# Kernel optimization log

Hardware: AMD Instinct MI355X
Metric: run time of the kernel (lower is better)

## Reference

```python
import jax, jax.numpy as jnp
import numpy as np
import math

B, S, HID = 2, 2048, 4096
NH, NKV = 32, 8
HD = HID // NH  # 128
ROPE_BASE = 10000.0


def _rope_tables(seq_len, dim, base=ROPE_BASE):
    # ntk_alpha = 1 and mscale = 1 for seq_len <= training_seqlen
    inv_freq = 1.0 / (base ** (jnp.arange(0, dim, 2, dtype=jnp.float32) / dim))
    t = jnp.arange(seq_len, dtype=jnp.float32)
    freqs = jnp.einsum('i,j->ij', t, inv_freq)          # [S, dim/2]
    emb = jnp.concatenate([freqs, freqs], axis=-1)       # [S, dim]
    return jnp.cos(emb), jnp.sin(emb)


def setup_inputs() -> dict:
    key = jax.random.key(0)
    ks = jax.random.split(key, 5)
    hidden_states = jax.random.normal(ks[0], (B, S, HID), dtype=jnp.float32)
    # additive causal mask [B, 1, S, S]
    causal = jnp.where(jnp.tril(jnp.ones((S, S), dtype=bool)), 0.0, -1e9)
    attention_mask = jnp.broadcast_to(causal[None, None], (B, 1, S, S)).astype(jnp.float32)
    cos, sin = _rope_tables(S, HD)
    sc = 0.02
    Wq = jax.random.normal(ks[1], (HID, HID), dtype=jnp.float32) * sc
    Wkv = jax.random.normal(ks[2], (2 * NKV * HD, HID), dtype=jnp.float32) * sc
    Wd = jax.random.normal(ks[3], (HID, HID), dtype=jnp.float32) * sc
    bd = jnp.zeros((HID,), dtype=jnp.float32)
    return {"hidden_states": hidden_states, "attention_mask": attention_mask,
            "cos": cos, "sin": sin, "Wq": Wq, "Wkv": Wkv, "Wd": Wd, "bd": bd}


def _rotate_half(x):
    x1, x2 = jnp.split(x, 2, axis=-1)
    return jnp.concatenate([-x2, x1], axis=-1)


def reference(hidden_states, attention_mask, cos, sin, Wq, Wkv, Wd, bd):
    bsz, seq_len, _ = hidden_states.shape
    # Q projection: [B,S,HID] -> [B,NH,S,HD]
    q = (hidden_states @ Wq.T).reshape(bsz, seq_len, NH, HD).transpose(0, 2, 1, 3)
    # fused KV projection: [B,S,NKV,2*HD] -> split -> [B,NKV,S,HD] each
    kv = (hidden_states @ Wkv.T).reshape(bsz, seq_len, NKV, 2 * HD)
    k, v = jnp.split(kv, 2, axis=-1)
    k = k.transpose(0, 2, 1, 3)
    v = v.transpose(0, 2, 1, 3)
    # RoPE (broadcast cos/sin [S,HD] over batch and heads)
    c = cos[None, None, :, :]
    s = sin[None, None, :, :]
    q = q * c + _rotate_half(q) * s
    k = k * c + _rotate_half(k) * s
    # repeat_kv: expand KV heads to NH heads (group size NH//NKV)
    n_rep = NH // NKV
    k = jnp.repeat(k, n_rep, axis=1)  # [B,NH,S,HD]
    v = jnp.repeat(v, n_rep, axis=1)
    # attention
    scores = jnp.einsum('bhqd,bhkd->bhqk', q, k) / math.sqrt(HD)
    scores = scores + attention_mask[:, :, :, :seq_len]
    probs = jax.nn.softmax(scores.astype(jnp.float32), axis=-1).astype(q.dtype)
    attn = jnp.einsum('bhqk,bhkd->bhqd', probs, v)
    attn = attn.transpose(0, 2, 1, 3).reshape(bsz, seq_len, HID)
    return attn @ Wd.T + bd
```

## Files before the change

kernel.cpp:

```cpp
#include <hip/hip_runtime.h>

typedef __bf16 bf16;
typedef __bf16 bf16x4 __attribute__((ext_vector_type(4)));
typedef __bf16 bf16x8 __attribute__((ext_vector_type(8)));
typedef float floatx4 __attribute__((ext_vector_type(4)));

static constexpr int B_ = 2, S_ = 2048, HID_ = 4096, NH_ = 32, NKV_ = 8, HD_ = 128;

__device__ __forceinline__ void gll16(const void* g, void* l) {
    __builtin_amdgcn_global_load_lds(
        (const __attribute__((address_space(1))) void*)g,
        (__attribute__((address_space(3))) void*)l, 16, 0, 0);
}

__device__ __forceinline__ bf16x8 cvt8(const float* p) {
    float4 f0 = *(const float4*)p;
    float4 f1 = *(const float4*)(p + 4);
    bf16x8 v;
    v[0] = (bf16)f0.x; v[1] = (bf16)f0.y; v[2] = (bf16)f0.z; v[3] = (bf16)f0.w;
    v[4] = (bf16)f1.x; v[5] = (bf16)f1.y; v[6] = (bf16)f1.z; v[7] = (bf16)f1.w;
    return v;
}

__global__ __launch_bounds__(256) void cvt_kernel(const float* __restrict__ in,
                                                  bf16* __restrict__ out, int n8)
{
    int i = blockIdx.x * 256 + threadIdx.x;
    if (i >= n8) return;
    ((bf16x8*)out)[i] = cvt8(in + (size_t)i * 8);
}

template<bool ABF, bool WBF, int EPI>
__global__ __launch_bounds__(256) void gemm_kernel(
    const void* __restrict__ Ap, const void* __restrict__ Wp,
    const float* __restrict__ bias, void* __restrict__ Cp,
    bf16* __restrict__ Kw, bf16* __restrict__ Vtw,
    int M, int N, int K)
{
    constexpr bool FAST = ABF && WBF;
    constexpr int STR = FAST ? 32 : 40;
    __shared__ __attribute__((aligned(16))) bf16 smem[2 * 128 * 40];
    bf16* Als = smem;
    bf16* Bls = smem + 128 * STR;

    const int tid = threadIdx.x;
    const int lane = tid & 63, wave = tid >> 6;
    const int lm = lane & 15, lq = lane >> 4;
    const int wr = (wave >> 1) * 64, wc = (wave & 1) * 64;
    const int m0 = blockIdx.y * 128, n0 = blockIdx.x * 128;

    floatx4 acc[4][4];
    #pragma unroll
    for (int i = 0; i < 4; i++)
        #pragma unroll
        for (int j = 0; j < 4; j++) acc[i][j] = (floatx4){0.f, 0.f, 0.f, 0.f};

    const int sr = tid >> 1;
    const int sc = (tid & 1) * 16;

    for (int k0 = 0; k0 < K; k0 += 32) {
        __syncthreads();
        if (FAST) {
            #pragma unroll
            for (int t = 0; t < 2; t++) {
                const int o = wave * 2048 + t * 1024 + lane * 16;
                const int row = o >> 6, ch = (o >> 4) & 3;
                const int ub = wave * 1024 + t * 512;
                gll16((const bf16*)Ap + (size_t)(m0 + row) * K + k0 + ch * 8, &Als[ub]);
                gll16((const bf16*)Wp + (size_t)(n0 + row) * K + k0 + ch * 8, &Bls[ub]);
            }
        } else {
            if (ABF) {
                const bf16* aptr = (const bf16*)Ap + (size_t)(m0 + sr) * K + sc + k0;
                *(bf16x8*)&Als[sr * STR + sc]     = *(const bf16x8*)(aptr);
                *(bf16x8*)&Als[sr * STR + sc + 8] = *(const bf16x8*)(aptr + 8);
            } else {
                const float* aptr = (const float*)Ap + (size_t)(m0 + sr) * K + sc + k0;
                *(bf16x8*)&Als[sr * STR + sc]     = cvt8(aptr);
                *(bf16x8*)&Als[sr * STR + sc + 8] = cvt8(aptr + 8);
            }
            const float* wptr = (const float*)Wp + (size_t)(n0 + sr) * K + sc + k0;
            *(bf16x8*)&Bls[sr * STR + sc]     = cvt8(wptr);
            *(bf16x8*)&Bls[sr * STR + sc + 8] = cvt8(wptr + 8);
        }
        __syncthreads();
        bf16x8 af[4], bfr[4];
        const int ko = lq * 8;
        #pragma unroll
        for (int i = 0; i < 4; i++) af[i]  = *(const bf16x8*)&Als[(wr + i * 16 + lm) * STR + ko];
        #pragma unroll
        for (int j = 0; j < 4; j++) bfr[j] = *(const bf16x8*)&Bls[(wc + j * 16 + lm) * STR + ko];
        #pragma unroll
        for (int i = 0; i < 4; i++)
            #pragma unroll
            for (int j = 0; j < 4; j++)
                acc[i][j] = __builtin_amdgcn_mfma_f32_16x16x32_bf16(af[i], bfr[j], acc[i][j], 0, 0, 0);
    }

    #pragma unroll
    for (int i = 0; i < 4; i++)
        #pragma unroll
        for (int j = 0; j < 4; j++) {
            const int col = n0 + wc + j * 16 + lm;
            const int row0 = m0 + wr + i * 16 + lq * 4;
            if (EPI == 0) {
                #pragma unroll
                for (int r = 0; r < 4; r++)
                    ((bf16*)Cp)[(size_t)(row0 + r) * N + col] = (bf16)acc[i][j][r];
            } else if (EPI == 1) {
                const float bv = bias ? bias[col] : 0.f;
                #pragma unroll
                for (int r = 0; r < 4; r++)
                    ((float*)Cp)[(size_t)(row0 + r) * N + col] = acc[i][j][r] + bv;
            } else {
                const int head = col >> 8, off = col & 255;
                const int b = row0 >> 11, s0 = row0 & (S_ - 1);
                if (off < HD_) {
                    bf16* kp = Kw + ((size_t)(b * NKV_ + head) * S_ + s0) * HD_ + off;
                    #pragma unroll
                    for (int r = 0; r < 4; r++) kp[(size_t)r * HD_] = (bf16)acc[i][j][r];
                } else {
                    bf16x4 pv;
                    #pragma unroll
                    for (int r = 0; r < 4; r++) pv[r] = (bf16)acc[i][j][r];
                    *(bf16x4*)&Vtw[((size_t)(b * NKV_ + head) * HD_ + (off - HD_)) * S_ + s0] = pv;
                }
            }
        }
}

__global__ __launch_bounds__(256) void rope_kernel(
    bf16* __restrict__ Qd, bf16* __restrict__ Kd,
    const float* __restrict__ cosd, const float* __restrict__ sind)
{
    const int idx = blockIdx.x * 256 + threadIdx.x;
    const int QROWS = B_ * S_ * NH_;
    const int d = idx & 63;
    const int row = idx >> 6;
    bf16* base; int s;
    if (row < QROWS) { base = Qd + (size_t)row * HD_; s = (row / NH_) & (S_ - 1); }
    else            { int rk = row - QROWS; base = Kd + (size_t)rk * HD_; s = rk & (S_ - 1); }
    const float c  = cosd[s * HD_ + d];
    const float sn = sind[s * HD_ + d];
    const float x1 = (float)base[d];
    const float x2 = (float)base[d + 64];
    base[d]      = (bf16)(x1 * c - x2 * sn);
    base[d + 64] = (bf16)(x2 * c + x1 * sn);
}

__global__ __launch_bounds__(256) void attn_kernel(
    const bf16* __restrict__ Q, const bf16* __restrict__ Kw,
    const bf16* __restrict__ Vtw, bf16* __restrict__ O)
{
    const int bq = (int)gridDim.x - 1 - (int)blockIdx.x;
    const int h = blockIdx.y, b = blockIdx.z;
    const int kh = h >> 2;
    const int tid = threadIdx.x, wave = tid >> 6, lane = tid & 63;
    const int lm = lane & 15, lq = lane >> 4;

    __shared__ __attribute__((aligned(16))) bf16 Kls[64 * 128];
    __shared__ __attribute__((aligned(16))) bf16 Vls[128 * 64];
    __shared__ __attribute__((aligned(16))) bf16 Pls[4][16 * 72];

    const int q0 = bq * 64 + wave * 16;
    bf16x8 qa[4];
    {
        const bf16* qb = Q + ((size_t)(b * S_ + q0 + lm) * NH_ + h) * HD_;
        #pragma unroll
        for (int ks = 0; ks < 4; ks++) qa[ks] = *(const bf16x8*)(qb + ks * 32 + lq * 8);
    }

    float l_i[4];
    floatx4 oacc[8];
    #pragma unroll
    for (int r = 0; r < 4; r++) l_i[r] = 0.f;
    #pragma unroll
    for (int ct = 0; ct < 8; ct++) oacc[ct] = (floatx4){0.f, 0.f, 0.f, 0.f};

    const float scale = 0.08838834764831845f;
    const bf16* Kbase = Kw  + (size_t)(b * NKV_ + kh) * S_ * HD_;
    const bf16* Vbase = Vtw + (size_t)(b * NKV_ + kh) * HD_ * S_;
    const int nkt = bq + 1;

    for (int it = 0; it < nkt; ++it) {
        const int kt = it * 64;
        __syncthreads();
        #pragma unroll
        for (int t = 0; t < 4; t++) {
            const int o = wave * 4096 + t * 1024 + lane * 16;
            const int ub = (wave * 4096 + t * 1024) / 2;
            { const int row = o >> 8, pos = (o >> 4) & 15, c = (pos - row) & 15;
              gll16(Kbase + (size_t)(kt + row) * HD_ + c * 8, &Kls[ub]); }
            { const int row = o >> 7, pos = (o >> 4) & 7, c = (pos - row) & 7;
              gll16(Vbase + (size_t)row * S_ + kt + c * 8, &Vls[ub]); }
        }
        __syncthreads();

        floatx4 sacc[4];
        #pragma unroll
        for (int nt = 0; nt < 4; nt++) sacc[nt] = (floatx4){0.f, 0.f, 0.f, 0.f};
        #pragma unroll
        for (int nt = 0; nt < 4; nt++) {
            const int key = nt * 16 + lm;
            #pragma unroll
            for (int ks = 0; ks < 4; ks++) {
                bf16x8 kf = *(const bf16x8*)&Kls[key * 128 + ((ks * 4 + lq + key) & 15) * 8];
                sacc[nt] = __builtin_amdgcn_mfma_f32_16x16x32_bf16(qa[ks], kf, sacc[nt], 0, 0, 0);
            }
        }

        #pragma unroll
        for (int r = 0; r < 4; r++) {
            const int qrow = q0 + lq * 4 + r;
            float lacc = 0.f;
            #pragma unroll
            for (int nt = 0; nt < 4; nt++) {
                const int kcol = kt + nt * 16 + lm;
                const float sv = sacc[nt][r] * scale + (kcol > qrow ? -1e9f : 0.f);
                const float p = __expf(sv - 20.0f);
                lacc += p;
                Pls[wave][(lq * 4 + r) * 72 + nt * 16 + lm] = (bf16)p;
            }
            l_i[r] += lacc;
        }

        #pragma unroll
        for (int ks2 = 0; ks2 < 2; ks2++) {
            bf16x8 pa = *(const bf16x8*)&Pls[wave][lm * 72 + ks2 * 32 + lq * 8];
            #pragma unroll
            for (int ct = 0; ct < 8; ct++) {
                const int dr = ct * 16 + lm;
                bf16x8 vb = *(const bf16x8*)&Vls[dr * 64 + ((ks2 * 4 + lq + dr) & 7) * 8];
                oacc[ct] = __builtin_amdgcn_mfma_f32_16x16x32_bf16(pa, vb, oacc[ct], 0, 0, 0);
            }
        }
    }

    #pragma unroll
    for (int r = 0; r < 4; r++) {
        float l = l_i[r];
        #pragma unroll
        for (int off = 1; off < 16; off <<= 1)
            l += __shfl_xor(l, off, 64);
        l_i[r] = l;
    }

    #pragma unroll
    for (int ct = 0; ct < 8; ct++)
        #pragma unroll
        for (int r = 0; r < 4; r++) {
            const int qrow = q0 + lq * 4 + r;
            O[(size_t)(b * S_ + qrow) * HID_ + h * HD_ + ct * 16 + lm]
                = (bf16)(oacc[ct][r] / l_i[r]);
        }
}

extern "C" void kernel_launch(void* const* d_in, const int* in_sizes, int n_in,
                              void* d_out, int out_size, void* d_ws, size_t ws_size,
                              hipStream_t stream)
{
    const float* hidden = (const float*)d_in[0];
    const float* cosd = (const float*)d_in[2];
    const float* sind = (const float*)d_in[3];
    const float* Wq   = (const float*)d_in[4];
    const float* Wkv  = (const float*)d_in[5];
    const float* Wd   = (const float*)d_in[6];
    const float* bd   = (const float*)d_in[7];
    float* out = (float*)d_out;

    const int M = B_ * S_;
    const int NKVC = 2 * NKV_ * HD_;
    bf16* Qw = (bf16*)d_out;
    bf16* wsb = (bf16*)d_ws;
    dim3 blk(256);

    const size_t E_HID  = (size_t)M * HID_;
    const size_t E_WKV  = (size_t)NKVC * HID_;
    const size_t E_K    = (size_t)B_ * NKV_ * S_ * HD_;
    const bool full = ws_size >= 2 * (3 * E_HID + E_WKV + 2 * E_K);

    const int rope_blocks = (B_ * S_ * NH_ + B_ * NKV_ * S_) * 64 / 256;

    if (full) {
        bf16* hb   = wsb;
        bf16* wqb  = hb   + E_HID;
        bf16* wkvb = wqb  + E_HID;
        bf16* wdb  = wkvb + E_WKV;
        bf16* Kw   = wdb  + E_HID;
        bf16* Vtw  = Kw   + E_K;
        bf16* Aw   = hb;

        cvt_kernel<<<dim3(E_HID / 8 / 256), blk, 0, stream>>>(hidden, hb,  (int)(E_HID / 8));
        cvt_kernel<<<dim3(E_HID / 8 / 256), blk, 0, stream>>>(Wq,     wqb, (int)(E_HID / 8));
        cvt_kernel<<<dim3(E_WKV / 8 / 256), blk, 0, stream>>>(Wkv,    wkvb,(int)(E_WKV / 8));
        cvt_kernel<<<dim3(E_HID / 8 / 256), blk, 0, stream>>>(Wd,     wdb, (int)(E_HID / 8));

        gemm_kernel<true, true, 0><<<dim3(HID_ / 128, M / 128), blk, 0, stream>>>(
            hb, wqb, nullptr, Qw, nullptr, nullptr, M, HID_, HID_);
        gemm_kernel<true, true, 2><<<dim3(NKVC / 128, M / 128), blk, 0, stream>>>(
            hb, wkvb, nullptr, nullptr, Kw, Vtw, M, NKVC, HID_);
        rope_kernel<<<dim3(rope_blocks), blk, 0, stream>>>(Qw, Kw, cosd, sind);
        attn_kernel<<<dim3(S_ / 64, NH_, B_), blk, 0, stream>>>(Qw, Kw, Vtw, Aw);
        gemm_kernel<true, true, 1><<<dim3(HID_ / 128, M / 128), blk, 0, stream>>>(
            Aw, wdb, bd, out, nullptr, nullptr, M, HID_, HID_);
    } else {
        bf16* Kw  = wsb;
        bf16* Vtw = Kw  + E_K;
        bf16* Aw  = Vtw + E_K;

        gemm_kernel<false, false, 0><<<dim3(HID_ / 128, M / 128), blk, 0, stream>>>(
            hidden, Wq, nullptr, Qw, nullptr, nullptr, M, HID_, HID_);
        gemm_kernel<false, false, 2><<<dim3(NKVC / 128, M / 128), blk, 0, stream>>>(
            hidden, Wkv, nullptr, nullptr, Kw, Vtw, M, NKVC, HID_);
        rope_kernel<<<dim3(rope_blocks), blk, 0, stream>>>(Qw, Kw, cosd, sind);
        attn_kernel<<<dim3(S_ / 64, NH_, B_), blk, 0, stream>>>(Qw, Kw, Vtw, Aw);
        gemm_kernel<true, false, 1><<<dim3(HID_ / 128, M / 128), blk, 0, stream>>>(
            Aw, Wd, bd, out, nullptr, nullptr, M, HID_, HID_);
    }
}
```

Baseline: 1.009 ms.

## Replace bf16 GEMMs with 256x256-tile, 4-stage pipelined 512-thread kernel

Adds a new GEMM kernel with 256x256 output tiles, 8 waves per block, and a 4-slot LDS ring buffer. Tiles are prefetched three K-steps ahead with direct global-to-LDS loads under explicit vmcnt waits, and MFMA phases are interleaved with loads under raised priority. The three projection GEMMs in the full-workspace path now use it, aiming to hide memory latency and increase per-block data reuse. In exchange it uses much more LDS and registers, and with fewer, larger blocks (for example 256 for the Q and output GEMMs) occupancy and tail balance may suffer.

```diff
diff --git a/kernel.cpp b/kernel.cpp
--- a/kernel.cpp
+++ b/kernel.cpp
@@ -30,75 +30,108 @@
     ((bf16x8*)out)[i] = cvt8(in + (size_t)i * 8);
 }
 
-template<bool ABF, bool WBF, int EPI>
-__global__ __launch_bounds__(256) void gemm_kernel(
-    const void* __restrict__ Ap, const void* __restrict__ Wp,
+template<int EPI>
+__global__ __launch_bounds__(512, 2) void gemm256_kernel(
+    const bf16* __restrict__ Ap, const bf16* __restrict__ Wp,
     const float* __restrict__ bias, void* __restrict__ Cp,
     bf16* __restrict__ Kw, bf16* __restrict__ Vtw,
     int M, int N, int K)
 {
-    constexpr bool FAST = ABF && WBF;
-    constexpr int STR = FAST ? 32 : 40;
-    __shared__ __attribute__((aligned(16))) bf16 smem[2 * 128 * 40];
-    bf16* Als = smem;
-    bf16* Bls = smem + 128 * STR;
+    __shared__ __attribute__((aligned(16))) bf16 As[4 * 8192];
+    __shared__ __attribute__((aligned(16))) bf16 Bs[4 * 8192];
 
     const int tid = threadIdx.x;
-    const int lane = tid & 63, wave = tid >> 6;
+    const int lane = tid & 63, wv = tid >> 6;
     const int lm = lane & 15, lq = lane >> 4;
-    const int wr = (wave >> 1) * 64, wc = (wave & 1) * 64;
-    const int m0 = blockIdx.y * 128, n0 = blockIdx.x * 128;
-
-    floatx4 acc[4][4];
-    #pragma unroll
-    for (int i = 0; i < 4; i++)
+    const int wr = (wv >> 2) * 128, wc = (wv & 3) * 64;
+    const int m0 = blockIdx.y * 256, n0 = blockIdx.x * 256;
+
+    const int NT = K >> 5;
+
+    const int sr = lane >> 2, sch = lane & 3;
+    const bf16* aA0 = Ap + (size_t)(m0 + wv * 32 +      sr) * K + sch * 8;
+    const bf16* aA1 = Ap + (size_t)(m0 + wv * 32 + 16 + sr) * K + sch * 8;
+    const bf16* aB0 = Wp + (size_t)(n0 + wv * 32 +      sr) * K + sch * 8;
+    const bf16* aB1 = Wp + (size_t)(n0 + wv * 32 + 16 + sr) * K + sch * 8;
+    const int ub0 = wv * 1024;
+    const int ub1 = wv * 1024 + 512;
+
+    floatx4 acc[8][4];
+    #pragma unroll
+    for (int i = 0; i < 8; i++)
         #pragma unroll
         for (int j = 0; j < 4; j++) acc[i][j] = (floatx4){0.f, 0.f, 0.f, 0.f};
 
-    const int sr = tid >> 1;
-    const int sc = (tid & 1) * 16;
-
-    for (int k0 = 0; k0 < K; k0 += 32) {
-        __syncthreads();
-        if (FAST) {
-            #pragma unroll
-            for (int t = 0; t < 2; t++) {
-                const int o = wave * 2048 + t * 1024 + lane * 16;
-                const int row = o >> 6, ch = (o >> 4) & 3;
-                const int ub = wave * 1024 + t * 512;
-                gll16((const bf16*)Ap + (size_t)(m0 + row) * K + k0 + ch * 8, &Als[ub]);
-                gll16((const bf16*)Wp + (size_t)(n0 + row) * K + k0 + ch * 8, &Bls[ub]);
-            }
-        } else {
-            if (ABF) {
-                const bf16* aptr = (const bf16*)Ap + (size_t)(m0 + sr) * K + sc + k0;
-                *(bf16x8*)&Als[sr * STR + sc]     = *(const bf16x8*)(aptr);
-                *(bf16x8*)&Als[sr * STR + sc + 8] = *(const bf16x8*)(aptr + 8);
-            } else {
-                const float* aptr = (const float*)Ap + (size_t)(m0 + sr) * K + sc + k0;
-                *(bf16x8*)&Als[sr * STR + sc]     = cvt8(aptr);
-                *(bf16x8*)&Als[sr * STR + sc + 8] = cvt8(aptr + 8);
-            }
-            const float* wptr = (const float*)Wp + (size_t)(n0 + sr) * K + sc + k0;
-            *(bf16x8*)&Bls[sr * STR + sc]     = cvt8(wptr);
-            *(bf16x8*)&Bls[sr * STR + sc + 8] = cvt8(wptr + 8);
-        }
-        __syncthreads();
+    #pragma unroll
+    for (int ts = 0; ts < 3; ++ts) {
+        if (ts < NT) {
+            const int sl = ts & 3;
+            const size_t ko = (size_t)ts * 32;
+            gll16(aA0 + ko, &As[sl * 8192 + ub0]);
+            gll16(aA1 + ko, &As[sl * 8192 + ub1]);
+            gll16(aB0 + ko, &Bs[sl * 8192 + ub0]);
+            gll16(aB1 + ko, &Bs[sl * 8192 + ub1]);
+        }
+    }
+    if (NT >= 3) asm volatile("s_waitcnt vmcnt(8)");
+    else         asm volatile("s_waitcnt vmcnt(0)");
+    __builtin_amdgcn_s_barrier();
+
+    for (int t = 0; t < NT; ++t) {
+        const bf16* Asl = As + (t & 3) * 8192;
+        const bf16* Bsl = Bs + (t & 3) * 8192;
+        const int ts = t + 3;
+        const int sl = ts & 3;
+        const bool st = ts < NT;
+        const size_t ko = (size_t)ts * 32;
+
         bf16x8 af[4], bfr[4];
-        const int ko = lq * 8;
-        #pragma unroll
-        for (int i = 0; i < 4; i++) af[i]  = *(const bf16x8*)&Als[(wr + i * 16 + lm) * STR + ko];
-        #pragma unroll
-        for (int j = 0; j < 4; j++) bfr[j] = *(const bf16x8*)&Bls[(wc + j * 16 + lm) * STR + ko];
+        #pragma unroll
+        for (int i = 0; i < 4; i++)
+            af[i] = *(const bf16x8*)&Asl[(wr + i * 16 + lm) * 32 + lq * 8];
+        #pragma unroll
+        for (int j = 0; j < 4; j++)
+            bfr[j] = *(const bf16x8*)&Bsl[(wc + j * 16 + lm) * 32 + lq * 8];
+        if (st) {
+            gll16(aA0 + ko, &As[sl * 8192 + ub0]);
+            gll16(aA1 + ko, &As[sl * 8192 + ub1]);
+        }
+        __builtin_amdgcn_s_barrier();
+        asm volatile("s_waitcnt lgkmcnt(0)");
+        __builtin_amdgcn_s_setprio(1);
         #pragma unroll
         for (int i = 0; i < 4; i++)
             #pragma unroll
             for (int j = 0; j < 4; j++)
                 acc[i][j] = __builtin_amdgcn_mfma_f32_16x16x32_bf16(af[i], bfr[j], acc[i][j], 0, 0, 0);
-    }
-
-    #pragma unroll
-    for (int i = 0; i < 4; i++)
+        __builtin_amdgcn_s_setprio(0);
+        __builtin_amdgcn_s_barrier();
+
+        bf16x8 af2[4];
+        #pragma unroll
+        for (int i = 0; i < 4; i++)
+            af2[i] = *(const bf16x8*)&Asl[(wr + 64 + i * 16 + lm) * 32 + lq * 8];
+        if (st) {
+            gll16(aB0 + ko, &Bs[sl * 8192 + ub0]);
+            gll16(aB1 + ko, &Bs[sl * 8192 + ub1]);
+        }
+        __builtin_amdgcn_s_barrier();
+        asm volatile("s_waitcnt lgkmcnt(0)");
+        __builtin_amdgcn_s_setprio(1);
+        #pragma unroll
+        for (int i = 0; i < 4; i++)
+            #pragma unroll
+            for (int j = 0; j < 4; j++)
+                acc[4 + i][j] = __builtin_amdgcn_mfma_f32_16x16x32_bf16(af2[i], bfr[j], acc[4 + i][j], 0, 0, 0);
+        __builtin_amdgcn_s_setprio(0);
+        if (t < NT - 3)       asm volatile("s_waitcnt vmcnt(8)");
+        else if (t == NT - 3) asm volatile("s_waitcnt vmcnt(4)");
+        else                  asm volatile("s_waitcnt vmcnt(0)");
+        __builtin_amdgcn_s_barrier();
+    }
+
+    #pragma unroll
+    for (int i = 0; i < 8; i++)
         #pragma unroll
         for (int j = 0; j < 4; j++) {
             const int col = n0 + wc + j * 16 + lm;
@@ -129,6 +162,105 @@
         }
 }
 
+template<bool ABF, bool WBF, int EPI>
+__global__ __launch_bounds__(256) void gemm_kernel(
+    const void* __restrict__ Ap, const void* __restrict__ Wp,
+    const float* __restrict__ bias, void* __restrict__ Cp,
+    bf16* __restrict__ Kw, bf16* __restrict__ Vtw,
+    int M, int N, int K)
+{
+    constexpr bool FAST = ABF && WBF;
+    constexpr int STR = FAST ? 32 : 40;
+    __shared__ __attribute__((aligned(16))) bf16 smem[2 * 128 * 40];
+    bf16* Als = smem;
+    bf16* Bls = smem + 128 * STR;
+
+    const int tid = threadIdx.x;
+    const int lane = tid & 63, wave = tid >> 6;
+    const int lm = lane & 15, lq = lane >> 4;
+    const int wr = (wave >> 1) * 64, wc = (wave & 1) * 64;
+    const int m0 = blockIdx.y * 128, n0 = blockIdx.x * 128;
+
+    floatx4 acc[4][4];
+    #pragma unroll
+    for (int i = 0; i < 4; i++)
+        #pragma unroll
+        for (int j = 0; j < 4; j++) acc[i][j] = (floatx4){0.f, 0.f, 0.f, 0.f};
+
+    const int sr = tid >> 1;
+    const int sc = (tid & 1) * 16;
+
+    for (int k0 = 0; k0 < K; k0 += 32) {
+        __syncthreads();
+        if (FAST) {
+            #pragma unroll
+            for (int t = 0; t < 2; t++) {
+                const int o = wave * 2048 + t * 1024 + lane * 16;
+                const int row = o >> 6, ch = (o >> 4) & 3;
+                const int ub = wave * 1024 + t * 512;
+                gll16((const bf16*)Ap + (size_t)(m0 + row) * K + k0 + ch * 8, &Als[ub]);
+                gll16((const bf16*)Wp + (size_t)(n0 + row) * K + k0 + ch * 8, &Bls[ub]);
+            }
+        } else {
+            if (ABF) {
+                const bf16* aptr = (const bf16*)Ap + (size_t)(m0 + sr) * K + sc + k0;
+                *(bf16x8*)&Als[sr * STR + sc]     = *(const bf16x8*)(aptr);
+                *(bf16x8*)&Als[sr * STR + sc + 8] = *(const bf16x8*)(aptr + 8);
+            } else {
+                const float* aptr = (const float*)Ap + (size_t)(m0 + sr) * K + sc + k0;
+                *(bf16x8*)&Als[sr * STR + sc]     = cvt8(aptr);
+                *(bf16x8*)&Als[sr * STR + sc + 8] = cvt8(aptr + 8);
+            }
+            const float* wptr = (const float*)Wp + (size_t)(n0 + sr) * K + sc + k0;
+            *(bf16x8*)&Bls[sr * STR + sc]     = cvt8(wptr);
+            *(bf16x8*)&Bls[sr * STR + sc + 8] = cvt8(wptr + 8);
+        }
+        __syncthreads();
+        bf16x8 af[4], bfr[4];
+        const int ko = lq * 8;
+        #pragma unroll
+        for (int i = 0; i < 4; i++) af[i]  = *(const bf16x8*)&Als[(wr + i * 16 + lm) * STR + ko];
+        #pragma unroll
+        for (int j = 0; j < 4; j++) bfr[j] = *(const bf16x8*)&Bls[(wc + j * 16 + lm) * STR + ko];
+        #pragma unroll
+        for (int i = 0; i < 4; i++)
+            #pragma unroll
+            for (int j = 0; j < 4; j++)
+                acc[i][j] = __builtin_amdgcn_mfma_f32_16x16x32_bf16(af[i], bfr[j], acc[i][j], 0, 0, 0);
+    }
+
+    #pragma unroll
+    for (int i = 0; i < 4; i++)
+        #pragma unroll
+        for (int j = 0; j < 4; j++) {
+            const int col = n0 + wc + j * 16 + lm;
+            const int row0 = m0 + wr + i * 16 + lq * 4;
+            if (EPI == 0) {
+                #pragma unroll
+                for (int r = 0; r < 4; r++)
+                    ((bf16*)Cp)[(size_t)(row0 + r) * N + col] = (bf16)acc[i][j][r];
+            } else if (EPI == 1) {
+                const float bv = bias ? bias[col] : 0.f;
+                #pragma unroll
+                for (int r = 0; r < 4; r++)
+                    ((float*)Cp)[(size_t)(row0 + r) * N + col] = acc[i][j][r] + bv;
+            } else {
+                const int head = col >> 8, off = col & 255;
+                const int b = row0 >> 11, s0 = row0 & (S_ - 1);
+                if (off < HD_) {
+                    bf16* kp = Kw + ((size_t)(b * NKV_ + head) * S_ + s0) * HD_ + off;
+                    #pragma unroll
+                    for (int r = 0; r < 4; r++) kp[(size_t)r * HD_] = (bf16)acc[i][j][r];
+                } else {
+                    bf16x4 pv;
+                    #pragma unroll
+                    for (int r = 0; r < 4; r++) pv[r] = (bf16)acc[i][j][r];
+                    *(bf16x4*)&Vtw[((size_t)(b * NKV_ + head) * HD_ + (off - HD_)) * S_ + s0] = pv;
+                }
+            }
+        }
+}
+
 __global__ __launch_bounds__(256) void rope_kernel(
     bf16* __restrict__ Qd, bf16* __restrict__ Kd,
     const float* __restrict__ cosd, const float* __restrict__ sind)
@@ -273,6 +405,7 @@
     bf16* Qw = (bf16*)d_out;
     bf16* wsb = (bf16*)d_ws;
     dim3 blk(256);
+    dim3 blk512(512);
 
     const size_t E_HID  = (size_t)M * HID_;
     const size_t E_WKV  = (size_t)NKVC * HID_;
@@ -295,13 +428,13 @@
         cvt_kernel<<<dim3(E_WKV / 8 / 256), blk, 0, stream>>>(Wkv,    wkvb,(int)(E_WKV / 8));
         cvt_kernel<<<dim3(E_HID / 8 / 256), blk, 0, stream>>>(Wd,     wdb, (int)(E_HID / 8));
 
-        gemm_kernel<true, true, 0><<<dim3(HID_ / 128, M / 128), blk, 0, stream>>>(
+        gemm256_kernel<0><<<dim3(HID_ / 256, M / 256), blk512, 0, stream>>>(
             hb, wqb, nullptr, Qw, nullptr, nullptr, M, HID_, HID_);
-        gemm_kernel<true, true, 2><<<dim3(NKVC / 128, M / 128), blk, 0, stream>>>(
+        gemm256_kernel<2><<<dim3(NKVC / 256, M / 256), blk512, 0, stream>>>(
             hb, wkvb, nullptr, nullptr, Kw, Vtw, M, NKVC, HID_);
         rope_kernel<<<dim3(rope_blocks), blk, 0, stream>>>(Qw, Kw, cosd, sind);
         attn_kernel<<<dim3(S_ / 64, NH_, B_), blk, 0, stream>>>(Qw, Kw, Vtw, Aw);
-        gemm_kernel<true, true, 1><<<dim3(HID_ / 128, M / 128), blk, 0, stream>>>(
+        gemm256_kernel<1><<<dim3(HID_ / 256, M / 256), blk512, 0, stream>>>(
             Aw, wdb, bd, out, nullptr, nullptr, M, HID_, HID_);
     } else {
         bf16* Kw  = wsb;
```

Result: faster. 888.8 us (-11.9%).
